# Optimization experiments

Measured on AMD Instinct MI355X. Metric: run time of the kernel, lower is better.

The kernel has to match this reference:

```python
import jax, jax.numpy as jnp
import numpy as np

N_EMBD = 1024
N_HEAD = 16
HEAD_DIM = N_EMBD // N_HEAD


def setup_inputs() -> dict:
    key = jax.random.key(0)
    k1, k2, k3, k4, k5 = jax.random.split(key, 5)
    scale = 1.0 / np.sqrt(N_EMBD)
    x = jax.random.normal(k1, (4, 2048, N_EMBD), dtype=jnp.float32)
    W_qkv = jax.random.normal(k2, (N_EMBD, 3 * N_EMBD), dtype=jnp.float32) * scale
    b_qkv = jax.random.normal(k3, (3 * N_EMBD,), dtype=jnp.float32) * 0.01
    W_proj = jax.random.normal(k4, (N_EMBD, N_EMBD), dtype=jnp.float32) * scale
    b_proj = jax.random.normal(k5, (N_EMBD,), dtype=jnp.float32) * 0.01
    return {"x": x, "W_qkv": W_qkv, "b_qkv": b_qkv, "W_proj": W_proj, "b_proj": b_proj}


def reference(x, W_qkv, b_qkv, W_proj, b_proj):
    B, T, C = x.shape
    qkv = x @ W_qkv + b_qkv                      # [B,T,3C]
    q, k, v = jnp.split(qkv, 3, axis=-1)
    # [B,T,C] -> [B,H,T,D]
    def to_heads(t):
        return t.reshape(B, T, N_HEAD, HEAD_DIM).transpose(0, 2, 1, 3)
    q, k, v = to_heads(q), to_heads(k), to_heads(v)
    att = jnp.einsum('bhqd,bhkd->bhqk', q, k) / np.sqrt(HEAD_DIM)
    causal = jnp.tril(jnp.ones((T, T), dtype=bool))
    att = jnp.where(causal, att, -jnp.inf)
    att = jax.nn.softmax(att, axis=-1)
    y = jnp.einsum('bhqk,bhkd->bhqd', att, v)    # [B,H,T,D]
    y = y.transpose(0, 2, 1, 3).reshape(B, T, C)
    return y @ W_proj + b_proj
```

## Files before the change

kernel.cpp:

```cpp
#include <hip/hip_runtime.h>
#include <hip/hip_bf16.h>
#include <cstdint>

#define B_   4
#define T_   2048
#define C_   1024
#define H_   16
#define D_   64
#define TC3  3072
#define M_   (B_ * T_)

typedef short  bf16x8 __attribute__((ext_vector_type(8)));
typedef float  f32x4  __attribute__((ext_vector_type(4)));

#define AS1(p) ((const __attribute__((address_space(1))) void*)(p))
#define AS3(p) ((__attribute__((address_space(3))) void*)(p))

__device__ inline float bf2f(unsigned short u) {
    union { unsigned int i; float f; } x; x.i = ((unsigned int)u) << 16; return x.f;
}
__device__ inline unsigned short f2bf(float f) {
    union { float f; unsigned int i; } x; x.f = f;
    return (unsigned short)((x.i + 0x7fffu + ((x.i >> 16) & 1u)) >> 16);
}

__global__ void cast_f32_bf16(const float* __restrict__ in,
                              unsigned short* __restrict__ out) {
    const size_t i = ((size_t)blockIdx.x * blockDim.x + threadIdx.x) * 8;
    f32x4 a = *(const f32x4*)(in + i);
    f32x4 b = *(const f32x4*)(in + i + 4);
    bf16x8 o;
#pragma unroll
    for (int j = 0; j < 4; ++j) { o[j] = (short)f2bf(a[j]); o[4 + j] = (short)f2bf(b[j]); }
    *(bf16x8*)(out + i) = o;
}

__global__ void transpose_cast(const float* __restrict__ in,
                               unsigned short* __restrict__ out, int R, int C) {
    __shared__ unsigned short tile[32][33];
    const int bc = blockIdx.x * 32, br = blockIdx.y * 32;
    const int tx = threadIdx.x & 31, ty = threadIdx.x >> 5;
#pragma unroll
    for (int i = 0; i < 4; ++i) {
        int r = ty + i * 8;
        tile[r][tx] = f2bf(in[(size_t)(br + r) * C + bc + tx]);
    }
    __syncthreads();
#pragma unroll
    for (int i = 0; i < 4; ++i) {
        int r = ty + i * 8;
        out[(size_t)(bc + r) * R + br + tx] = tile[tx][r];
    }
}

template <bool OUTF32>
__global__ __launch_bounds__(256, 2) void gemm_bt_bias(
    const unsigned short* __restrict__ A, const unsigned short* __restrict__ Bt,
    const float* __restrict__ bias, void* __restrict__ Cout,
    int M, int N, int K) {
    __shared__ unsigned short As[128 * 32];
    __shared__ unsigned short Bs[128 * 32];
    const int tid = threadIdx.x;
    const int wave = tid >> 6, lane = tid & 63;
    const int m0 = blockIdx.x * 128, n0 = blockIdx.y * 128;
    const int wr = (wave >> 1) * 64, wc = (wave & 1) * 64;

    f32x4 acc[4][4] = {};

    const int srow = (lane >> 2);
    const int scol = (lane & 3) * 8;

    for (int k0 = 0; k0 < K; k0 += 32) {
#pragma unroll
        for (int j = 0; j < 2; ++j) {
            const int chunk = wave * 2 + j;
            const int row = chunk * 16 + srow;
            __builtin_amdgcn_global_load_lds(
                AS1(A + (size_t)(m0 + row) * K + k0 + scol),
                AS3(As + chunk * 512), 16, 0, 0);
            __builtin_amdgcn_global_load_lds(
                AS1(Bt + (size_t)(n0 + row) * K + k0 + scol),
                AS3(Bs + chunk * 512), 16, 0, 0);
        }
        __syncthreads();
        bf16x8 a[4], b[4];
#pragma unroll
        for (int i = 0; i < 4; ++i)
            a[i] = *(const bf16x8*)&As[(wr + i * 16 + (lane & 15)) * 32 + (lane >> 4) * 8];
#pragma unroll
        for (int i = 0; i < 4; ++i)
            b[i] = *(const bf16x8*)&Bs[(wc + i * 16 + (lane & 15)) * 32 + (lane >> 4) * 8];
        __builtin_amdgcn_s_setprio(1);
#pragma unroll
        for (int i = 0; i < 4; ++i)
#pragma unroll
            for (int j = 0; j < 4; ++j)
                acc[i][j] = __builtin_amdgcn_mfma_f32_16x16x32_bf16(a[i], b[j], acc[i][j], 0, 0, 0);
        __builtin_amdgcn_s_setprio(0);
        __syncthreads();
    }

#pragma unroll
    for (int i = 0; i < 4; ++i) {
        const int rowb = m0 + wr + i * 16 + (lane >> 4) * 4;
#pragma unroll
        for (int j = 0; j < 4; ++j) {
            const int col = n0 + wc + j * 16 + (lane & 15);
            const float bv = bias[col];
#pragma unroll
            for (int r = 0; r < 4; ++r) {
                const float v = acc[i][j][r] + bv;
                if (OUTF32)
                    ((float*)Cout)[(size_t)(rowb + r) * N + col] = v;
                else
                    ((unsigned short*)Cout)[(size_t)(rowb + r) * N + col] = f2bf(v);
            }
        }
    }
}

__global__ __launch_bounds__(512, 4) void attn_kernel(
    const unsigned short* __restrict__ QKV, unsigned short* __restrict__ Y) {
    __shared__ unsigned short Kl[64][72];
    __shared__ unsigned short Vt[64][72];
    __shared__ unsigned short Pl[8][16][72];

    const int tid = threadIdx.x, wave = tid >> 6, lane = tid & 63;
    const int bh = blockIdx.x;
    const int pr = blockIdx.y;
    const int b = bh >> 4, h = bh & 15;
    const size_t rowbase = (size_t)b * T_ * TC3;
    const int l15 = lane & 15, lhi = lane >> 4;
    const int srow = tid >> 3;
    const int sseg = tid & 7;

    for (int sp = 0; sp < 2; ++sp) {
        const int tq = sp ? (15 - pr) : pr;
        const int qb = tq * 128;
        const int q0 = qb + wave * 16;
        const int ntiles = 2 * tq + 2;

        bf16x8 qf[2];
        {
            const unsigned short* p =
                QKV + rowbase + (size_t)(q0 + l15) * TC3 + h * 64 + lhi * 8;
            qf[0] = *(const bf16x8*)p;
            qf[1] = *(const bf16x8*)(p + 32);
#pragma unroll
            for (int hf = 0; hf < 2; ++hf)
#pragma unroll
                for (int j = 0; j < 8; ++j)
                    qf[hf][j] = (short)f2bf(bf2f((unsigned short)qf[hf][j]) * 0.18033688011f);
        }

        float m2[4], l_run[4];
        f32x4 o[4] = {};
#pragma unroll
        for (int r = 0; r < 4; ++r) { m2[r] = -1e30f; l_run[r] = 0.f; }

        __syncthreads();
        {
            const unsigned short* src =
                QKV + rowbase + (size_t)srow * TC3 + C_ + h * 64 + sseg * 8;
            bf16x8 k8 = *(const bf16x8*)src;
            bf16x8 v8 = *(const bf16x8*)(src + C_);
            *(bf16x8*)&Kl[srow][sseg * 8] = k8;
            const int swz = srow ^ (sseg << 3);
#pragma unroll
            for (int j = 0; j < 8; ++j)
                Vt[sseg * 8 + j][swz] = (unsigned short)v8[j];
        }

        for (int t = 0; t < ntiles; ++t) {
            const int kv0 = t * 64;
            __syncthreads();

            bf16x8 pk8, pv8;
            const bool pf_valid = (t + 1 < ntiles);
            if (pf_valid) {
                const unsigned short* src =
                    QKV + rowbase + (size_t)(kv0 + 64 + srow) * TC3 + C_ + h * 64 + sseg * 8;
                pk8 = *(const bf16x8*)src;
                pv8 = *(const bf16x8*)(src + C_);
            }

            if (q0 + 15 >= kv0) {
                f32x4 s[4];
                __builtin_amdgcn_s_setprio(1);
#pragma unroll
                for (int kt = 0; kt < 4; ++kt) {
                    bf16x8 kf0 = *(const bf16x8*)&Kl[kt * 16 + l15][lhi * 8];
                    bf16x8 kf1 = *(const bf16x8*)&Kl[kt * 16 + l15][32 + lhi * 8];
                    f32x4 acc = {};
                    acc = __builtin_amdgcn_mfma_f32_16x16x32_bf16(qf[0], kf0, acc, 0, 0, 0);
                    acc = __builtin_amdgcn_mfma_f32_16x16x32_bf16(qf[1], kf1, acc, 0, 0, 0);
                    s[kt] = acc;
                }
                __builtin_amdgcn_s_setprio(0);

                const bool needmask = (kv0 + 63 > q0);
                if (needmask) {
#pragma unroll
                    for (int kt = 0; kt < 4; ++kt) {
                        const int kcol = kv0 + kt * 16 + l15;
#pragma unroll
                        for (int r = 0; r < 4; ++r) {
                            const int q = q0 + lhi * 4 + r;
                            s[kt][r] = (kcol <= q) ? s[kt][r] : -1e30f;
                        }
                    }
                }
                float tmax[4];
#pragma unroll
                for (int r = 0; r < 4; ++r)
                    tmax[r] = fmaxf(fmaxf(s[0][r], s[1][r]), fmaxf(s[2][r], s[3][r]));
#pragma unroll
                for (int msk = 1; msk < 16; msk <<= 1)
#pragma unroll
                    for (int r = 0; r < 4; ++r)
                        tmax[r] = fmaxf(tmax[r], __shfl_xor(tmax[r], msk, 64));

                bool exc = false;
#pragma unroll
                for (int r = 0; r < 4; ++r)
                    exc = exc || (tmax[r] > m2[r] + 11.5416f);
                if (__any(exc)) {
#pragma unroll
                    for (int r = 0; r < 4; ++r) {
                        const float mnew = fmaxf(m2[r], tmax[r]);
                        const float corr = exp2f(m2[r] - mnew);
                        m2[r] = mnew;
                        l_run[r] *= corr;
#pragma unroll
                        for (int dt = 0; dt < 4; ++dt) o[dt][r] *= corr;
                    }
                }
                float tsum[4] = {0.f, 0.f, 0.f, 0.f};
#pragma unroll
                for (int kt = 0; kt < 4; ++kt)
#pragma unroll
                    for (int r = 0; r < 4; ++r) {
                        const float p = exp2f(s[kt][r] - m2[r]);
                        s[kt][r] = p;
                        tsum[r] += p;
                    }
#pragma unroll
                for (int msk = 1; msk < 16; msk <<= 1)
#pragma unroll
                    for (int r = 0; r < 4; ++r)
                        tsum[r] += __shfl_xor(tsum[r], msk, 64);
#pragma unroll
                for (int r = 0; r < 4; ++r) l_run[r] += tsum[r];

#pragma unroll
                for (int kt = 0; kt < 4; ++kt)
#pragma unroll
                    for (int r = 0; r < 4; ++r)
                        Pl[wave][lhi * 4 + r][kt * 16 + l15] = f2bf(s[kt][r]);

                bf16x8 pf0 = *(const bf16x8*)&Pl[wave][l15][lhi * 8];
                bf16x8 pf1 = *(const bf16x8*)&Pl[wave][l15][32 + lhi * 8];
                __builtin_amdgcn_s_setprio(1);
#pragma unroll
                for (int dt = 0; dt < 4; ++dt) {
                    const int d = dt * 16 + l15;
                    const int xs = (d >> 3) << 3;
                    bf16x8 vf0 = *(const bf16x8*)&Vt[d][(lhi * 8) ^ xs];
                    bf16x8 vf1 = *(const bf16x8*)&Vt[d][(32 + lhi * 8) ^ xs];
                    o[dt] = __builtin_amdgcn_mfma_f32_16x16x32_bf16(pf0, vf0, o[dt], 0, 0, 0);
                    o[dt] = __builtin_amdgcn_mfma_f32_16x16x32_bf16(pf1, vf1, o[dt], 0, 0, 0);
                }
                __builtin_amdgcn_s_setprio(0);
            }

            __syncthreads();
            if (pf_valid) {
                *(bf16x8*)&Kl[srow][sseg * 8] = pk8;
                const int swz = srow ^ (sseg << 3);
#pragma unroll
                for (int j = 0; j < 8; ++j)
                    Vt[sseg * 8 + j][swz] = (unsigned short)pv8[j];
            }
        }

#pragma unroll
        for (int dt = 0; dt < 4; ++dt)
#pragma unroll
            for (int r = 0; r < 4; ++r) {
                const int q = q0 + lhi * 4 + r;
                const int d = dt * 16 + l15;
                Y[((size_t)b * T_ + q) * C_ + h * 64 + d] = f2bf(o[dt][r] / l_run[r]);
            }
    }
}

extern "C" void kernel_launch(void* const* d_in, const int* in_sizes, int n_in,
                              void* d_out, int out_size, void* d_ws, size_t ws_size,
                              hipStream_t stream) {
    const float* x     = (const float*)d_in[0];
    const float* Wqkv  = (const float*)d_in[1];
    const float* bqkv  = (const float*)d_in[2];
    const float* Wproj = (const float*)d_in[3];
    const float* bproj = (const float*)d_in[4];
    float* out = (float*)d_out;

    char* ws = (char*)d_ws;
    unsigned short* qkv    = (unsigned short*)(ws);
    unsigned short* yat    = (unsigned short*)(ws + 50331648);
    unsigned short* WqkvT  = (unsigned short*)(ws + 67108864);
    unsigned short* WprojT = (unsigned short*)(ws + 73400320);
    unsigned short* xb     = (unsigned short*)(ws + 75497472);

    cast_f32_bf16<<<dim3((M_ * C_) / (256 * 8)), dim3(256), 0, stream>>>(x, xb);
    transpose_cast<<<dim3(TC3 / 32, C_ / 32), dim3(256), 0, stream>>>(Wqkv, WqkvT, C_, TC3);
    transpose_cast<<<dim3(C_ / 32, C_ / 32), dim3(256), 0, stream>>>(Wproj, WprojT, C_, C_);
    gemm_bt_bias<false><<<dim3(M_ / 128, TC3 / 128), dim3(256), 0, stream>>>(xb, WqkvT, bqkv, qkv, M_, TC3, C_);
    attn_kernel<<<dim3(B_ * H_, 8), dim3(512), 0, stream>>>(qkv, yat);
    gemm_bt_bias<true><<<dim3(M_ / 128, C_ / 128), dim3(256), 0, stream>>>(yat, WprojT, bproj, out, M_, C_, C_);
}
```

Baseline: 224.7 us.

## Compute transposed scores so P feeds PV MFMA from registers, skipping LDS

The QK^T MFMA operands are swapped so each lane holds scores for a single query column. The probabilities can then be packed with v_cvt_pk_bf16 straight into the A-operand layout of a 16x16x16 MFMA, which removes the per-wave P staging buffer in LDS and its write/read round trip. Softmax max/sum now need only two cross-lane shuffles instead of four per row, and the row stats are kept as scalars and broadcast with __shfl when rescaling the output. In exchange, the PV product uses twice as many MFMA instructions of the smaller K=16 shape, which may have lower per-instruction throughput on this hardware.

Result: faster. 183.6 us (-18.3%).

```diff
diff --git a/kernel.cpp b/kernel.cpp
--- a/kernel.cpp
+++ b/kernel.cpp
@@ -11,6 +11,7 @@
 #define M_   (B_ * T_)
 
 typedef short  bf16x8 __attribute__((ext_vector_type(8)));
+typedef short  bf16x4 __attribute__((ext_vector_type(4)));
 typedef float  f32x4  __attribute__((ext_vector_type(4)));
 
 #define AS1(p) ((const __attribute__((address_space(1))) void*)(p))
@@ -22,6 +23,19 @@
 __device__ inline unsigned short f2bf(float f) {
     union { float f; unsigned int i; } x; x.f = f;
     return (unsigned short)((x.i + 0x7fffu + ((x.i >> 16) & 1u)) >> 16);
+}
+__device__ inline unsigned int cvtpk_bf16(float a, float b) {
+    unsigned int r;
+    asm("v_cvt_pk_bf16_f32 %0, %1, %2" : "=v"(r) : "v"(a), "v"(b));
+    return r;
+}
+__device__ inline f32x4 mfma16x16x16(bf16x4 a, bf16x4 b, f32x4 c) {
+#if __has_builtin(__builtin_amdgcn_mfma_f32_16x16x16bf16_1k)
+    return __builtin_amdgcn_mfma_f32_16x16x16bf16_1k(a, b, c, 0, 0, 0);
+#else
+    asm("v_mfma_f32_16x16x16_bf16 %0, %1, %2, %0" : "+v"(c) : "v"(a), "v"(b));
+    return c;
+#endif
 }
 
 __global__ void cast_f32_bf16(const float* __restrict__ in,
@@ -123,7 +137,6 @@
     const unsigned short* __restrict__ QKV, unsigned short* __restrict__ Y) {
     __shared__ unsigned short Kl[64][72];
     __shared__ unsigned short Vt[64][72];
-    __shared__ unsigned short Pl[8][16][72];
 
     const int tid = threadIdx.x, wave = tid >> 6, lane = tid & 63;
     const int bh = blockIdx.x;
@@ -139,6 +152,7 @@
         const int qb = tq * 128;
         const int q0 = qb + wave * 16;
         const int ntiles = 2 * tq + 2;
+        const int qv = q0 + l15;
 
         bf16x8 qf[2];
         {
@@ -153,10 +167,8 @@
                     qf[hf][j] = (short)f2bf(bf2f((unsigned short)qf[hf][j]) * 0.18033688011f);
         }
 
-        float m2[4], l_run[4];
+        float m2 = -1e30f, l_run = 0.f;
         f32x4 o[4] = {};
-#pragma unroll
-        for (int r = 0; r < 4; ++r) { m2[r] = -1e30f; l_run[r] = 0.f; }
 
         __syncthreads();
         {
@@ -192,8 +204,8 @@
                     bf16x8 kf0 = *(const bf16x8*)&Kl[kt * 16 + l15][lhi * 8];
                     bf16x8 kf1 = *(const bf16x8*)&Kl[kt * 16 + l15][32 + lhi * 8];
                     f32x4 acc = {};
-                    acc = __builtin_amdgcn_mfma_f32_16x16x32_bf16(qf[0], kf0, acc, 0, 0, 0);
-                    acc = __builtin_amdgcn_mfma_f32_16x16x32_bf16(qf[1], kf1, acc, 0, 0, 0);
+                    acc = __builtin_amdgcn_mfma_f32_16x16x32_bf16(kf0, qf[0], acc, 0, 0, 0);
+                    acc = __builtin_amdgcn_mfma_f32_16x16x32_bf16(kf1, qf[1], acc, 0, 0, 0);
                     s[kt] = acc;
                 }
                 __builtin_amdgcn_s_setprio(0);
@@ -202,73 +214,71 @@
                 if (needmask) {
 #pragma unroll
                     for (int kt = 0; kt < 4; ++kt) {
-                        const int kcol = kv0 + kt * 16 + l15;
-#pragma unroll
-                        for (int r = 0; r < 4; ++r) {
-                            const int q = q0 + lhi * 4 + r;
-                            s[kt][r] = (kcol <= q) ? s[kt][r] : -1e30f;
-                        }
+                        const int kb = kv0 + kt * 16 + lhi * 4;
+#pragma unroll
+                        for (int r = 0; r < 4; ++r)
+                            s[kt][r] = (kb + r <= qv) ? s[kt][r] : -1e30f;
                     }
                 }
-                float tmax[4];
+                f32x4 vm = s[0];
 #pragma unroll
                 for (int r = 0; r < 4; ++r)
-                    tmax[r] = fmaxf(fmaxf(s[0][r], s[1][r]), fmaxf(s[2][r], s[3][r]));
-#pragma unroll
-                for (int msk = 1; msk < 16; msk <<= 1)
+                    vm[r] = fmaxf(fmaxf(s[0][r], s[1][r]), fmaxf(s[2][r], s[3][r]));
+                float tmax = fmaxf(fmaxf(vm[0], vm[1]), fmaxf(vm[2], vm[3]));
+                tmax = fmaxf(tmax, __shfl_xor(tmax, 16, 64));
+                tmax = fmaxf(tmax, __shfl_xor(tmax, 32, 64));
+
+                if (__any(tmax > m2 + 11.5416f)) {
+                    const float mnew = fmaxf(m2, tmax);
+                    const float corr = exp2f(m2 - mnew);
+                    m2 = mnew; l_run *= corr;
+                    float cq[4];
 #pragma unroll
                     for (int r = 0; r < 4; ++r)
-                        tmax[r] = fmaxf(tmax[r], __shfl_xor(tmax[r], msk, 64));
-
-                bool exc = false;
-#pragma unroll
-                for (int r = 0; r < 4; ++r)
-                    exc = exc || (tmax[r] > m2[r] + 11.5416f);
-                if (__any(exc)) {
+                        cq[r] = __shfl(corr, lhi * 16 + lhi * 4 + r, 64);
+#pragma unroll
+                    for (int dt = 0; dt < 4; ++dt)
+#pragma unroll
+                        for (int r = 0; r < 4; ++r) o[dt][r] *= cq[r];
+                }
+                float tsum = 0.f;
+#pragma unroll
+                for (int kt = 0; kt < 4; ++kt) {
 #pragma unroll
                     for (int r = 0; r < 4; ++r) {
-                        const float mnew = fmaxf(m2[r], tmax[r]);
-                        const float corr = exp2f(m2[r] - mnew);
-                        m2[r] = mnew;
-                        l_run[r] *= corr;
-#pragma unroll
-                        for (int dt = 0; dt < 4; ++dt) o[dt][r] *= corr;
+                        const float p = exp2f(s[kt][r] - m2);
+                        s[kt][r] = p;
                     }
                 }
-                float tsum[4] = {0.f, 0.f, 0.f, 0.f};
-#pragma unroll
-                for (int kt = 0; kt < 4; ++kt)
-#pragma unroll
-                    for (int r = 0; r < 4; ++r) {
-                        const float p = exp2f(s[kt][r] - m2[r]);
-                        s[kt][r] = p;
-                        tsum[r] += p;
-                    }
-#pragma unroll
-                for (int msk = 1; msk < 16; msk <<= 1)
+                {
+                    f32x4 vs;
 #pragma unroll
                     for (int r = 0; r < 4; ++r)
-                        tsum[r] += __shfl_xor(tsum[r], msk, 64);
-#pragma unroll
-                for (int r = 0; r < 4; ++r) l_run[r] += tsum[r];
-
-#pragma unroll
-                for (int kt = 0; kt < 4; ++kt)
-#pragma unroll
-                    for (int r = 0; r < 4; ++r)
-                        Pl[wave][lhi * 4 + r][kt * 16 + l15] = f2bf(s[kt][r]);
-
-                bf16x8 pf0 = *(const bf16x8*)&Pl[wave][l15][lhi * 8];
-                bf16x8 pf1 = *(const bf16x8*)&Pl[wave][l15][32 + lhi * 8];
+                        vs[r] = (s[0][r] + s[1][r]) + (s[2][r] + s[3][r]);
+                    tsum = (vs[0] + vs[1]) + (vs[2] + vs[3]);
+                    tsum += __shfl_xor(tsum, 16, 64);
+                    tsum += __shfl_xor(tsum, 32, 64);
+                    l_run += tsum;
+                }
+                bf16x4 pa[4];
+#pragma unroll
+                for (int kt = 0; kt < 4; ++kt) {
+                    unsigned int w0 = cvtpk_bf16(s[kt][0], s[kt][1]);
+                    unsigned int w1 = cvtpk_bf16(s[kt][2], s[kt][3]);
+                    unsigned int pw[2] = { w0, w1 };
+                    pa[kt] = *(const bf16x4*)pw;
+                }
+
                 __builtin_amdgcn_s_setprio(1);
 #pragma unroll
                 for (int dt = 0; dt < 4; ++dt) {
                     const int d = dt * 16 + l15;
                     const int xs = (d >> 3) << 3;
-                    bf16x8 vf0 = *(const bf16x8*)&Vt[d][(lhi * 8) ^ xs];
-                    bf16x8 vf1 = *(const bf16x8*)&Vt[d][(32 + lhi * 8) ^ xs];
-                    o[dt] = __builtin_amdgcn_mfma_f32_16x16x32_bf16(pf0, vf0, o[dt], 0, 0, 0);
-                    o[dt] = __builtin_amdgcn_mfma_f32_16x16x32_bf16(pf1, vf1, o[dt], 0, 0, 0);
+#pragma unroll
+                    for (int kt = 0; kt < 4; ++kt) {
+                        bf16x4 vb = *(const bf16x4*)&Vt[d][(kt * 16 + lhi * 4) ^ xs];
+                        o[dt] = mfma16x16x16(pa[kt], vb, o[dt]);
+                    }
                 }
                 __builtin_amdgcn_s_setprio(0);
             }
@@ -283,13 +293,19 @@
             }
         }
 
+        float rq[4];
+#pragma unroll
+        for (int r = 0; r < 4; ++r) {
+            const float lq = __shfl(l_run, lhi * 16 + lhi * 4 + r, 64);
+            rq[r] = 1.0f / lq;
+        }
 #pragma unroll
         for (int dt = 0; dt < 4; ++dt)
 #pragma unroll
             for (int r = 0; r < 4; ++r) {
                 const int q = q0 + lhi * 4 + r;
                 const int d = dt * 16 + l15;
-                Y[((size_t)b * T_ + q) * C_ + h * 64 + d] = f2bf(o[dt][r] / l_run[r]);
+                Y[((size_t)b * T_ + q) * C_ + h * 64 + d] = f2bf(o[dt][r] * rq[r]);
             }
     }
 }
```
